# Kernel tuning notes

Hardware: AMD Instinct MI355X
Metric: run time of the kernel (lower is better)

Reference implementation:

```python
import jax, jax.numpy as jnp
import numpy as np

N, Wd = 1000000, 20
EPS = 1e-16


def setup_inputs() -> dict:
    key = jax.random.key(0)
    ks = jax.random.split(key, 40)
    def rn(i, shape, scale=0.05):
        return jax.random.normal(ks[i], shape, dtype=jnp.float32) * scale
    inp = {
        "X": rn(0, (1, 14), 1.0),
        "read_weights": jax.nn.sigmoid(rn(1, (1, N), 1.0)),
        "write_weights": jax.nn.sigmoid(rn(2, (1, N), 1.0)),
        "Memory": jnp.full((N, Wd), 1e-6, dtype=jnp.float32),
        "read_head": jax.nn.sigmoid(rn(3, (1, Wd), 1.0)),
        "W1": rn(4, (48, 14)), "b1": rn(5, (48,)),
        "W2": rn(6, (72, 48)), "b2": rn(7, (72,)),
        "Wxi": rn(8, ((Wd + 6) * 2 + 2 * Wd, 72)), "bxi": rn(9, ((Wd + 6) * 2 + 2 * Wd,)),
        "Wz": rn(10, (3, 72)), "bz": rn(11, (3,)),
        "Wv": rn(12, (20, 325)), "bv": rn(13, (20,)),
        "aW1": rn(14, (110, 40)), "ab1": rn(15, (110,)),
        "aW2": rn(16, (190, 110)), "ab2": rn(17, (190,)),
        "aW3": rn(18, (270, 190)), "ab3": rn(19, (270,)),
        "aW4": rn(20, (325, 270)), "ab4": rn(21, (325,)),
        "mW1": rn(22, (110, 40)), "mb1": rn(23, (110,)),
        "mW2": rn(24, (190, 110)), "mb2": rn(25, (190,)),
        "mW3": rn(26, (270, 190)), "mb3": rn(27, (270,)),
        "mW4": rn(28, (325, 270)), "mb4": rn(29, (325,)),
    }
    return inp


def _alu(x, W1, b1, W2, b2, W3, b3, W4, b4):
    x = jax.nn.relu(x @ W1.T + b1)
    x = jax.nn.relu(x @ W2.T + b2)
    x = jax.nn.relu(x @ W3.T + b3)
    return jax.nn.softmax(x @ W4.T + b4, axis=-1)


def _head_params(p):  # p: (1, Wd+6)
    k = jnp.tanh(p[0, :Wd])[None, :]              # (1, Wd)
    g = jax.nn.sigmoid(p[0, Wd])
    s = jax.nn.softmax(p[0, Wd + 1:Wd + 4])        # (3,)
    gamma = 1.0 + jax.nn.softplus(p[0, Wd + 4])
    beta = jax.nn.softplus(p[0, Wd + 5])
    return k, g, s, gamma, beta


def _address(Memory, k, beta, g, s, gamma, w_prev):
    Me = Memory + EPS                              # (N, Wd)
    ke = k + EPS                                   # (1, Wd)
    num = (Me @ ke.T)[:, 0]                        # (N,)
    den = jnp.maximum(jnp.linalg.norm(Me, axis=-1), 1e-8) * \
          jnp.maximum(jnp.linalg.norm(ke, axis=-1), 1e-8)
    w_c = jax.nn.softmax((num / den) * beta)       # (N,)
    w_g = g * w_c + (1.0 - g) * w_prev             # (1, N)
    pad = jnp.concatenate([w_g[:, -1:], w_g, w_g[:, :1]], axis=1)  # (1, N+2)
    w_r = s[0] * pad[:, :N] + s[1] * pad[:, 1:N + 1] + s[2] * pad[:, 2:]
    w = w_r ** gamma
    return w / (jnp.sum(w, axis=1, keepdims=True) + EPS)


def reference(X, read_weights, write_weights, Memory, read_head,
              W1, b1, W2, b2, Wxi, bxi, Wz, bz, Wv, bv,
              aW1, ab1, aW2, ab2, aW3, ab3, aW4, ab4,
              mW1, mb1, mW2, mb2, mW3, mb3, mW4, mb4):
    h = X @ W1.T + b1                # (1, 48)  (no activation, faithful)
    h = h @ W2.T + b2                # (1, 72)
    xi = h @ Wxi.T + bxi             # (1, 92)
    zeta = h @ Wz.T + bz             # (1, 3)

    rp = xi[0, :Wd + 6][None, :]
    wp = xi[0, Wd + 6:(Wd + 6) * 2][None, :]
    erase = jax.nn.sigmoid(xi[0, (Wd + 6) * 2:(Wd + 6) * 2 + Wd][None, :])
    add = jnp.tanh(xi[0, (Wd + 6) * 2 + Wd:(Wd + 6) * 2 + 2 * Wd][None, :])

    k, g, s, gamma, beta = _head_params(rp)
    rw = _address(Memory, k, beta, g, s, gamma, read_weights)
    k, g, s, gamma, beta = _head_params(wp)
    ww = _address(Memory, k, beta, g, s, gamma, write_weights)

    new_read_head = rw @ Memory                    # (1, Wd)
    alu_in = jnp.concatenate([read_head, new_read_head], axis=1)  # (1, 2*Wd)

    rho = jax.nn.sigmoid(zeta[0, 0])
    alu_head = jax.nn.softmax(zeta[:, 1:], axis=-1)  # (1, 2)
    out_add = _alu(alu_in, aW1, ab1, aW2, ab2, aW3, ab3, aW4, ab4)
    out_mul = _alu(alu_in, mW1, mb1, mW2, mb2, mW3, mb3, mW4, mb4)
    out = alu_head[0, 0] * out_add + alu_head[0, 1] * out_mul  # (1, 325)

    v = out @ Wv.T + bv                              # (1, 20)
    add = rho * add + (1.0 - rho) * v

    new_memory = Memory * (1.0 - ww.T @ erase) + ww.T @ add  # (N, Wd)
    return out, rw, ww, new_memory, new_read_head
```

## Files before the change

kernel.cpp:

```cpp
#include <hip/hip_runtime.h>
#include <math.h>

#define NN 1000000
#define NF4 5000000
#define WD 20
#define NB 977
#define PST 1024

#define OUT_OFF 0
#define RW_OFF  325
#define WW_OFF  1000325
#define NM_OFF  2000325
#define NRH_OFF 22000325

__device__ __forceinline__ float sigmoidf_(float x){ return 1.0f/(1.0f+expf(-x)); }
__device__ __forceinline__ float softplusf_(float x){ return (x>30.f)?x:log1pf(expf(x)); }

__global__ __launch_bounds__(256) void k_scores(
    const float* __restrict__ X,
    const float* __restrict__ W1, const float* __restrict__ b1,
    const float* __restrict__ W2, const float* __restrict__ b2,
    const float* __restrict__ Wxi, const float* __restrict__ bxi,
    const float* __restrict__ Wz, const float* __restrict__ bz,
    const float* __restrict__ M, float* __restrict__ Pg,
    float2* __restrict__ sc2, float4* __restrict__ pms){
  __shared__ float4 ld[1280];
  __shared__ float h1[48], h2[72], xi[95], sP[132];
  int t=threadIdx.x, b=blockIdx.x;
  if(t<48){ float a=b1[t]; const float* w=W1+t*14; for(int c=0;c<14;c++) a+=X[c]*w[c]; h1[t]=a; }
  __syncthreads();
  if(t<72){ float a=b2[t]; const float* w=W2+t*48; for(int c=0;c<48;c++) a+=h1[c]*w[c]; h2[t]=a; }
  __syncthreads();
  if(t<92){ float a=bxi[t]; const float* w=Wxi+t*72; for(int c=0;c<72;c++) a+=h2[c]*w[c]; xi[t]=a; }
  else if(t<95){ int z=t-92; float a=bz[z]; const float* w=Wz+z*72; for(int c=0;c<72;c++) a+=h2[c]*w[c]; xi[92+z]=a; }
  __syncthreads();
  if(t<20){
    sP[0+t]  = tanhf(xi[t]);
    sP[32+t] = tanhf(xi[26+t]);
    sP[64+t] = sigmoidf_(xi[52+t]);
    sP[84+t] = tanhf(xi[72+t]);
  }
  __syncthreads();
  if(t==32){
    float g=sigmoidf_(xi[20]);
    float a0=xi[21],a1=xi[22],a2=xi[23];
    float mx=fmaxf(a0,fmaxf(a1,a2));
    float e0=expf(a0-mx),e1=expf(a1-mx),e2=expf(a2-mx),es=e0+e1+e2;
    float gamma=1.0f+softplusf_(xi[24]);
    float beta=softplusf_(xi[25]);
    float n2=0.f;
#pragma unroll
    for(int j=0;j<20;j++){ float ke=sP[j]+1e-16f; n2+=ke*ke; }
    sP[20]=g; sP[21]=e0/es; sP[22]=e1/es; sP[23]=e2/es; sP[24]=gamma; sP[25]=beta;
    sP[26]=fmaxf(sqrtf(n2),1e-8f);
  }
  if(t==96){
    float g=sigmoidf_(xi[46]);
    float a0=xi[47],a1=xi[48],a2=xi[49];
    float mx=fmaxf(a0,fmaxf(a1,a2));
    float e0=expf(a0-mx),e1=expf(a1-mx),e2=expf(a2-mx),es=e0+e1+e2;
    float gamma=1.0f+softplusf_(xi[50]);
    float beta=softplusf_(xi[51]);
    float n2=0.f;
#pragma unroll
    for(int j=0;j<20;j++){ float ke=sP[32+j]+1e-16f; n2+=ke*ke; }
    sP[52]=g; sP[53]=e0/es; sP[54]=e1/es; sP[55]=e2/es; sP[56]=gamma; sP[57]=beta;
    sP[58]=fmaxf(sqrtf(n2),1e-8f);
  }
  if(t==160){
    sP[104]=sigmoidf_(xi[92]);
    float mx=fmaxf(xi[93],xi[94]);
    float e1=expf(xi[93]-mx), e2=expf(xi[94]-mx);
    sP[105]=e1/(e1+e2); sP[106]=e2/(e1+e2);
  }
  __syncthreads();
  if(b==0 && t<132) Pg[t]=sP[t];
  float kr[20], kw[20];
#pragma unroll
  for(int j=0;j<20;j++){ kr[j]=sP[j]+1e-16f; kw[j]=sP[32+j]+1e-16f; }
  float betar=sP[25], betaw=sP[57], knr=sP[26], knw=sP[58];
  const float4* Mf4=(const float4*)M;
  float sR[4], sW[4];
  for(int p=0;p<4;p++){
    int rb=b*1024+p*256;
    size_t f4b=(size_t)rb*5;
#pragma unroll
    for(int k=0;k<5;k++){
      size_t idx=f4b+(size_t)(k*256+t);
      ld[k*256+t] = (idx<NF4)?Mf4[idx]:make_float4(0.f,0.f,0.f,0.f);
    }
    __syncthreads();
    int i=rb+t;
    float srv=-3.0e38f, swv=-3.0e38f;
    if(i<NN){
      float dr=0.f,dw=0.f,n2=0.f;
#pragma unroll
      for(int q=0;q<5;q++){
        float4 v=ld[t*5+q];
        float m0=v.x+1e-16f,m1=v.y+1e-16f,m2=v.z+1e-16f,m3=v.w+1e-16f;
        dr+=m0*kr[4*q]+m1*kr[4*q+1]+m2*kr[4*q+2]+m3*kr[4*q+3];
        dw+=m0*kw[4*q]+m1*kw[4*q+1]+m2*kw[4*q+2]+m3*kw[4*q+3];
        n2+=m0*m0+m1*m1+m2*m2+m3*m3;
      }
      float nm=fmaxf(sqrtf(n2),1e-8f);
      srv=betar*(dr/(nm*knr));
      swv=betaw*(dw/(nm*knw));
      sc2[i]=make_float2(srv,swv);
    }
    sR[p]=srv; sW[p]=swv;
    __syncthreads();
  }
  float* r1=(float*)ld; float* r2=r1+256;
  double* d1=(double*)(r1+512); double* d2=d1+256;
  float lm1=fmaxf(fmaxf(sR[0],sR[1]),fmaxf(sR[2],sR[3]));
  float lm2=fmaxf(fmaxf(sW[0],sW[1]),fmaxf(sW[2],sW[3]));
  r1[t]=lm1; r2[t]=lm2; __syncthreads();
  for(int o=128;o>0;o>>=1){ if(t<o){ r1[t]=fmaxf(r1[t],r1[t+o]); r2[t]=fmaxf(r2[t],r2[t+o]); } __syncthreads(); }
  float mb1=r1[0], mb2=r2[0]; __syncthreads();
  double s1=0.0,s2=0.0;
#pragma unroll
  for(int p=0;p<4;p++){ s1+=(double)expf(sR[p]-mb1); s2+=(double)expf(sW[p]-mb2); }
  d1[t]=s1; d2[t]=s2; __syncthreads();
  for(int o=128;o>0;o>>=1){ if(t<o){ d1[t]+=d1[t+o]; d2[t]+=d2[t+o]; } __syncthreads(); }
  if(t==0) pms[b]=make_float4(mb1,mb2,(float)d1[0],(float)d2[0]);
}

__global__ __launch_bounds__(256) void k_shift(const float2* __restrict__ sc2,
                        const float* __restrict__ wpr, const float* __restrict__ wpw,
                        const float* __restrict__ M, const float* __restrict__ P,
                        const float4* __restrict__ pms,
                        float* __restrict__ w_r_out, float* __restrict__ w_w_out,
                        double* __restrict__ pZ, double* __restrict__ pnrhT){
  __shared__ float4 ld[1280];
  __shared__ float bmS[4];
  float* r1=(float*)ld; float* r2=r1+256;
  double* d1=(double*)(r1+512); double* d2=d1+256;
  float* wsum=(float*)(d2+256);
  int t=threadIdx.x, b=blockIdx.x;
  float4 v4[4];
#pragma unroll
  for(int k=0;k<4;k++){
    int idx=t+k*256;
    v4[k] = (idx<NB) ? pms[idx] : make_float4(-3.0e38f,-3.0e38f,0.f,0.f);
  }
  float lm1=fmaxf(fmaxf(v4[0].x,v4[1].x),fmaxf(v4[2].x,v4[3].x));
  float lm2=fmaxf(fmaxf(v4[0].y,v4[1].y),fmaxf(v4[2].y,v4[3].y));
  r1[t]=lm1; r2[t]=lm2; __syncthreads();
  for(int o=128;o>0;o>>=1){ if(t<o){ r1[t]=fmaxf(r1[t],r1[t+o]); r2[t]=fmaxf(r2[t],r2[t+o]); } __syncthreads(); }
  if(t==0){ bmS[0]=r1[0]; bmS[1]=r2[0]; } __syncthreads();
  float mr=bmS[0], mw=bmS[1];
  double s1=0.0,s2=0.0;
#pragma unroll
  for(int k=0;k<4;k++){
    s1 += (double)v4[k].z * (double)expf(v4[k].x-mr);
    s2 += (double)v4[k].w * (double)expf(v4[k].y-mw);
  }
  d1[t]=s1; d2[t]=s2; __syncthreads();
  for(int o=128;o>0;o>>=1){ if(t<o){ d1[t]+=d1[t+o]; d2[t]+=d2[t+o]; } __syncthreads(); }
  if(t==0){ bmS[2]=(float)d1[0]; bmS[3]=(float)d2[0]; } __syncthreads();
  float Sr=bmS[2], Sw=bmS[3];
  float gr=P[20], s0r=P[21], s1r=P[22], s2r=P[23], gar=P[24];
  float gw=P[52], s0w=P[53], s1w=P[54], s2w=P[55], gaw=P[56];
  float omgr=1.0f-gr, omgw=1.0f-gw;
  const float4* Mf4=(const float4*)M;
  float acc[20];
#pragma unroll
  for(int j=0;j<20;j++) acc[j]=0.f;
  double zr=0.0, zw=0.0;
  for(int p=0;p<4;p++){
    int rb=b*1024+p*256;
    size_t f4b=(size_t)rb*5;
#pragma unroll
    for(int k=0;k<5;k++){
      size_t idx=f4b+(size_t)(k*256+t);
      ld[k*256+t] = (idx<NF4)?Mf4[idx]:make_float4(0.f,0.f,0.f,0.f);
    }
    __syncthreads();
    int i=rb+t;
    if(i<NN){
      int im1=(i==0)?(NN-1):(i-1);
      int ip1=(i==NN-1)?0:(i+1);
      float2 scm=sc2[im1], sc0=sc2[i], scp=sc2[ip1];
      float wgrm = gr*(expf(scm.x-mr)/Sr) + omgr*wpr[im1];
      float wgr0 = gr*(expf(sc0.x-mr)/Sr) + omgr*wpr[i  ];
      float wgrp = gr*(expf(scp.x-mr)/Sr) + omgr*wpr[ip1];
      float wgwm = gw*(expf(scm.y-mw)/Sw) + omgw*wpw[im1];
      float wgw0 = gw*(expf(sc0.y-mw)/Sw) + omgw*wpw[i  ];
      float wgwp = gw*(expf(scp.y-mw)/Sw) + omgw*wpw[ip1];
      float wr = powf(s0r*wgrm + s1r*wgr0 + s2r*wgrp, gar);
      float ww = powf(s0w*wgwm + s1w*wgw0 + s2w*wgwp, gaw);
      w_r_out[i]=wr; w_w_out[i]=ww;
      zr+=(double)wr; zw+=(double)ww;
#pragma unroll
      for(int q=0;q<5;q++){
        float4 mv=ld[t*5+q];
        acc[4*q+0]+=wr*mv.x; acc[4*q+1]+=wr*mv.y; acc[4*q+2]+=wr*mv.z; acc[4*q+3]+=wr*mv.w;
      }
    }
    __syncthreads();
  }
  d1[t]=zr; d2[t]=zw; __syncthreads();
  for(int o=128;o>0;o>>=1){ if(t<o){ d1[t]+=d1[t+o]; d2[t]+=d2[t+o]; } __syncthreads(); }
  if(t==0){ pZ[2*b]=d1[0]; pZ[2*b+1]=d2[0]; }
  __syncthreads();
#pragma unroll
  for(int j=0;j<20;j++){
    for(int off=32;off>0;off>>=1) acc[j]+=__shfl_down(acc[j],off,64);
  }
  int wave=t>>6, lane=t&63;
  if(lane==0){
#pragma unroll
    for(int j=0;j<20;j++) wsum[wave*20+j]=acc[j];
  }
  __syncthreads();
  if(t<20){
    double s=(double)wsum[0*20+t]+(double)wsum[1*20+t]+(double)wsum[2*20+t]+(double)wsum[3*20+t];
    pnrhT[(size_t)t*PST+b]=s;
  }
}

__global__ __launch_bounds__(256) void k_l12(
    const double* __restrict__ pZ, const double* __restrict__ pnrhT,
    const float* __restrict__ read_head,
    const float* __restrict__ aW1,const float* __restrict__ ab1,
    const float* __restrict__ mW1,const float* __restrict__ mb1,
    const float* __restrict__ aW2,const float* __restrict__ ab2,
    const float* __restrict__ mW2,const float* __restrict__ mb2,
    float* __restrict__ out, float* __restrict__ h2g, double* __restrict__ Sd){
  __shared__ float in40[40], h1s[110];
  __shared__ double dred[24];
  int t=threadIdx.x, b=blockIdx.x, wave=t>>6, lane=t&63;
  int net=(b>=48);
  for(int j=wave; j<22; j+=4){
    double s=0.0;
    if(j<20){
      const double* src=pnrhT+(size_t)j*PST;
      for(int idx=lane; idx<NB; idx+=64) s+=src[idx];
    } else {
      for(int idx=lane; idx<NB; idx+=64) s+=pZ[2*idx+(j-20)];
    }
    for(int off=32;off>0;off>>=1) s+=__shfl_down(s,off,64);
    if(lane==0) dred[j]=s;
  }
  __syncthreads();
  if(t<20){
    double Zr=dred[20]+1e-16;
    float nv=(float)(dred[t]/Zr);
    in40[20+t]=nv; in40[t]=read_head[t];
    if(b==0) out[NRH_OFF+t]=nv;
  }
  if(b==0 && t==21){ Sd[0]=dred[20]; Sd[1]=dred[21]; }
  __syncthreads();
  int g=t>>4, l16=t&15;
  const float* W1=net?mW1:aW1; const float* B1=net?mb1:ab1;
  for(int pass=0; pass<7; ++pass){
    int r=pass*16+g;
    if(r<110){
      const float* w=W1+(size_t)r*40;
      float a=0.f;
      for(int c=l16;c<40;c+=16) a+=w[c]*in40[c];
      a+=__shfl_xor(a,8,64); a+=__shfl_xor(a,4,64); a+=__shfl_xor(a,2,64); a+=__shfl_xor(a,1,64);
      if(l16==0) h1s[r]=fmaxf(a+B1[r],0.f);
    }
  }
  __syncthreads();
  int r=(b-net*48)*4+wave;
  if(r<190){
    const float* w=(net?mW2:aW2)+(size_t)r*110;
    float a=0.f;
    for(int c=lane;c<110;c+=64) a+=w[c]*h1s[c];
    for(int off=32;off>0;off>>=1) a+=__shfl_down(a,off,64);
    if(lane==0) h2g[net*190+r]=fmaxf(a+(net?mb2:ab2)[r],0.f);
  }
}

__global__ __launch_bounds__(256) void k_l3(const float* __restrict__ h2g,
    const float* __restrict__ aW3,const float* __restrict__ ab3,
    const float* __restrict__ mW3,const float* __restrict__ mb3,
    float* __restrict__ h3g){
  int t=threadIdx.x, b=blockIdx.x, wave=t>>6, lane=t&63;
  int net=(b>=68);
  int r=(b-net*68)*4+wave;
  if(r>=270) return;
  const float* w=(net?mW3:aW3)+(size_t)r*190;
  const float* in=h2g+net*190;
  float a=0.f;
  for(int c=lane;c<190;c+=64) a+=w[c]*in[c];
  for(int off=32;off>0;off>>=1) a+=__shfl_down(a,off,64);
  if(lane==0) h3g[net*270+r]=fmaxf(a+(net?mb3:ab3)[r],0.f);
}

__global__ __launch_bounds__(256) void k_l4(const float* __restrict__ h3g,
    const float* __restrict__ aW4,const float* __restrict__ ab4,
    const float* __restrict__ mW4,const float* __restrict__ mb4,
    float* __restrict__ h4g){
  int t=threadIdx.x, b=blockIdx.x, wave=t>>6, lane=t&63;
  int net=(b>=82);
  int r=(b-net*82)*4+wave;
  if(r>=325) return;
  const float* w=(net?mW4:aW4)+(size_t)r*270;
  const float* in=h3g+net*270;
  float a=0.f;
  for(int c=lane;c<270;c+=64) a+=w[c]*in[c];
  for(int off=32;off>0;off>>=1) a+=__shfl_down(a,off,64);
  if(lane==0) h4g[net*325+r]=a+(net?mb4:ab4)[r];
}

__global__ __launch_bounds__(256) void k_fin(const float* __restrict__ h4g,
    const float* __restrict__ Wv, const float* __restrict__ bv,
    float* __restrict__ P, float* __restrict__ out){
  __shared__ float red[256], outv[325], sc[2];
  int t=threadIdx.x, b=blockIdx.x;
  float a0=h4g[t], a1=(t<69)?h4g[256+t]:-3.0e38f;
  red[t]=fmaxf(a0,a1); __syncthreads();
  for(int o=128;o>0;o>>=1){ if(t<o) red[t]=fmaxf(red[t],red[t+o]); __syncthreads(); }
  if(t==0) sc[0]=red[0]; __syncthreads();
  float ea0=expf(a0-sc[0]), ea1=(t<69)?expf(a1-sc[0]):0.f;
  red[t]=ea0+ea1; __syncthreads();
  for(int o=128;o>0;o>>=1){ if(t<o) red[t]+=red[t+o]; __syncthreads(); }
  if(t==0) sc[1]=red[0]; __syncthreads();
  float sA=sc[1];
  float pA0=ea0/sA, pA1=ea1/sA;
  __syncthreads();
  float m0=h4g[325+t], m1=(t<69)?h4g[325+256+t]:-3.0e38f;
  red[t]=fmaxf(m0,m1); __syncthreads();
  for(int o=128;o>0;o>>=1){ if(t<o) red[t]=fmaxf(red[t],red[t+o]); __syncthreads(); }
  if(t==0) sc[0]=red[0]; __syncthreads();
  float em0=expf(m0-sc[0]), em1=(t<69)?expf(m1-sc[0]):0.f;
  red[t]=em0+em1; __syncthreads();
  for(int o=128;o>0;o>>=1){ if(t<o) red[t]+=red[t+o]; __syncthreads(); }
  if(t==0) sc[1]=red[0]; __syncthreads();
  float sM=sc[1];
  float ah0=P[105], ah1=P[106];
  outv[t]=ah0*pA0+ah1*(em0/sM);
  if(t<69) outv[256+t]=ah0*pA1+ah1*(em1/sM);
  __syncthreads();
  if(b==20){
    out[OUT_OFF+t]=outv[t];
    if(t<69) out[OUT_OFF+256+t]=outv[256+t];
  } else {
    const float* w=Wv+(size_t)b*325;
    float a=w[t]*outv[t];
    if(t<69) a+=w[256+t]*outv[256+t];
    red[t]=a; __syncthreads();
    for(int o=128;o>0;o>>=1){ if(t<o) red[t]+=red[t+o]; __syncthreads(); }
    if(t==0){
      float rho=P[104];
      P[112+b]=rho*P[84+b]+(1.0f-rho)*(red[0]+bv[b]);
    }
  }
}

__global__ __launch_bounds__(256) void k_memupd(const float* __restrict__ M,
                         float* __restrict__ w_r, float* __restrict__ w_w,
                         const float* __restrict__ P, const double* __restrict__ Sd,
                         float* __restrict__ nm){
  __shared__ float4 ld[1280];
  int t=threadIdx.x, b=blockIdx.x;
  float er[20], af[20];
#pragma unroll
  for(int j=0;j<20;j++){ er[j]=P[64+j]; af[j]=P[112+j]; }
  float Zr=(float)Sd[0]+1e-16f, Zw=(float)Sd[1]+1e-16f;
  const float4* Mf4=(const float4*)M;
  float4* nmf4=(float4*)nm;
  for(int p=0;p<4;p++){
    int rb=b*1024+p*256;
    size_t f4b=(size_t)rb*5;
#pragma unroll
    for(int k=0;k<5;k++){
      size_t idx=f4b+(size_t)(k*256+t);
      if(idx<NF4) ld[k*256+t]=Mf4[idx];
    }
    __syncthreads();
    int i=rb+t;
    if(i<NN){
      float wrn=w_r[i]/Zr;
      float wwn=w_w[i]/Zw;
      w_r[i]=wrn; w_w[i]=wwn;
#pragma unroll
      for(int q=0;q<5;q++){
        float4 v=ld[t*5+q];
        float4 o;
        o.x=v.x*(1.0f-wwn*er[4*q+0])+wwn*af[4*q+0];
        o.y=v.y*(1.0f-wwn*er[4*q+1])+wwn*af[4*q+1];
        o.z=v.z*(1.0f-wwn*er[4*q+2])+wwn*af[4*q+2];
        o.w=v.w*(1.0f-wwn*er[4*q+3])+wwn*af[4*q+3];
        ld[t*5+q]=o;
      }
    }
    __syncthreads();
#pragma unroll
    for(int k=0;k<5;k++){
      size_t idx=f4b+(size_t)(k*256+t);
      if(idx<NF4) nmf4[idx]=ld[k*256+t];
    }
    __syncthreads();
  }
}

extern "C" void kernel_launch(void* const* d_in, const int* in_sizes, int n_in,
                              void* d_out, int out_size, void* d_ws, size_t ws_size,
                              hipStream_t stream) {
  const float* X    =(const float*)d_in[0];
  const float* rwp  =(const float*)d_in[1];
  const float* wwp  =(const float*)d_in[2];
  const float* Mem  =(const float*)d_in[3];
  const float* rhd  =(const float*)d_in[4];
  const float* W1   =(const float*)d_in[5];
  const float* b1   =(const float*)d_in[6];
  const float* W2   =(const float*)d_in[7];
  const float* b2   =(const float*)d_in[8];
  const float* Wxi  =(const float*)d_in[9];
  const float* bxi  =(const float*)d_in[10];
  const float* Wz   =(const float*)d_in[11];
  const float* bz   =(const float*)d_in[12];
  const float* Wv   =(const float*)d_in[13];
  const float* bv   =(const float*)d_in[14];
  const float* aW1  =(const float*)d_in[15];
  const float* ab1  =(const float*)d_in[16];
  const float* aW2  =(const float*)d_in[17];
  const float* ab2  =(const float*)d_in[18];
  const float* aW3  =(const float*)d_in[19];
  const float* ab3  =(const float*)d_in[20];
  const float* aW4  =(const float*)d_in[21];
  const float* ab4  =(const float*)d_in[22];
  const float* mW1  =(const float*)d_in[23];
  const float* mb1  =(const float*)d_in[24];
  const float* mW2  =(const float*)d_in[25];
  const float* mb2  =(const float*)d_in[26];
  const float* mW3  =(const float*)d_in[27];
  const float* mb3  =(const float*)d_in[28];
  const float* mW4  =(const float*)d_in[29];
  const float* mb4  =(const float*)d_in[30];

  float* out = (float*)d_out;
  char* ws = (char*)d_ws;
  float*  P   = (float*)(ws + 0);
  double* Sd  = (double*)(ws + 2048);
  float*  h2g = (float*)(ws + 4096);
  float*  h3g = (float*)(ws + 8192);
  float*  h4g = (float*)(ws + 12288);
  float4* pms = (float4*)(ws + 16384);
  double* pZ  = (double*)(ws + 65536);
  double* pnrhT=(double*)(ws + 131072);

  float2* sc2 = (float2*)(out + NM_OFF);
  float*  w_r = out + RW_OFF;
  float*  w_w = out + WW_OFF;
  float*  nm  = out + NM_OFF;

  k_scores<<<NB,256,0,stream>>>(X,W1,b1,W2,b2,Wxi,bxi,Wz,bz,Mem,P,sc2,pms);
  k_shift<<<NB,256,0,stream>>>(sc2,rwp,wwp,Mem,P,pms,w_r,w_w,pZ,pnrhT);
  k_l12<<<96,256,0,stream>>>(pZ,pnrhT,rhd,aW1,ab1,mW1,mb1,aW2,ab2,mW2,mb2,out,h2g,Sd);
  k_l3<<<136,256,0,stream>>>(h2g,aW3,ab3,mW3,mb3,h3g);
  k_l4<<<164,256,0,stream>>>(h3g,aW4,ab4,mW4,mb4,h4g);
  k_fin<<<21,256,0,stream>>>(h4g,Wv,bv,P,out);
  k_memupd<<<NB,256,0,stream>>>(Mem,w_r,w_w,P,Sd,nm);
}
```

Baseline: 130.5 us.

## Fuse small MLP kernels into one cooperative kernel with grid syncs

Replaces the four small kernels (l12, l3, l4, fin) with a single cooperative kernel of 160 blocks that uses grid.sync between layers. This targets the launch overhead and inter-kernel gaps on the serial tail of the computation. It also spreads the first-layer work and the reductions across more waves. Grid-wide barriers carry their own cost, and layer 4 now loops over 650 rows with 640 waves.

After: 193.0 us. 48.0% more time.

```diff
diff --git a/kernel.cpp b/kernel.cpp
--- a/kernel.cpp
+++ b/kernel.cpp
@@ -1,11 +1,15 @@
 #include <hip/hip_runtime.h>
+#include <hip/hip_cooperative_groups.h>
 #include <math.h>
+
+namespace cg = cooperative_groups;
 
 #define NN 1000000
 #define NF4 5000000
 #define WD 20
 #define NB 977
 #define PST 1024
+#define CB 160
 
 #define OUT_OFF 0
 #define RW_OFF  325
@@ -219,134 +223,124 @@
   }
 }
 
-__global__ __launch_bounds__(256) void k_l12(
+__global__ __launch_bounds__(256) void k_coop(
     const double* __restrict__ pZ, const double* __restrict__ pnrhT,
-    const float* __restrict__ read_head,
+    const float* __restrict__ rhd,
     const float* __restrict__ aW1,const float* __restrict__ ab1,
     const float* __restrict__ mW1,const float* __restrict__ mb1,
     const float* __restrict__ aW2,const float* __restrict__ ab2,
     const float* __restrict__ mW2,const float* __restrict__ mb2,
-    float* __restrict__ out, float* __restrict__ h2g, double* __restrict__ Sd){
-  __shared__ float in40[40], h1s[110];
-  __shared__ double dred[24];
-  int t=threadIdx.x, b=blockIdx.x, wave=t>>6, lane=t&63;
-  int net=(b>=48);
-  for(int j=wave; j<22; j+=4){
-    double s=0.0;
-    if(j<20){
-      const double* src=pnrhT+(size_t)j*PST;
-      for(int idx=lane; idx<NB; idx+=64) s+=src[idx];
-    } else {
-      for(int idx=lane; idx<NB; idx+=64) s+=pZ[2*idx+(j-20)];
-    }
-    for(int off=32;off>0;off>>=1) s+=__shfl_down(s,off,64);
-    if(lane==0) dred[j]=s;
-  }
-  __syncthreads();
-  if(t<20){
-    double Zr=dred[20]+1e-16;
-    float nv=(float)(dred[t]/Zr);
-    in40[20+t]=nv; in40[t]=read_head[t];
-    if(b==0) out[NRH_OFF+t]=nv;
-  }
-  if(b==0 && t==21){ Sd[0]=dred[20]; Sd[1]=dred[21]; }
-  __syncthreads();
-  int g=t>>4, l16=t&15;
-  const float* W1=net?mW1:aW1; const float* B1=net?mb1:ab1;
-  for(int pass=0; pass<7; ++pass){
-    int r=pass*16+g;
-    if(r<110){
-      const float* w=W1+(size_t)r*40;
-      float a=0.f;
-      for(int c=l16;c<40;c+=16) a+=w[c]*in40[c];
-      a+=__shfl_xor(a,8,64); a+=__shfl_xor(a,4,64); a+=__shfl_xor(a,2,64); a+=__shfl_xor(a,1,64);
-      if(l16==0) h1s[r]=fmaxf(a+B1[r],0.f);
-    }
-  }
-  __syncthreads();
-  int r=(b-net*48)*4+wave;
-  if(r<190){
-    const float* w=(net?mW2:aW2)+(size_t)r*110;
-    float a=0.f;
-    for(int c=lane;c<110;c+=64) a+=w[c]*h1s[c];
-    for(int off=32;off>0;off>>=1) a+=__shfl_down(a,off,64);
-    if(lane==0) h2g[net*190+r]=fmaxf(a+(net?mb2:ab2)[r],0.f);
-  }
-}
-
-__global__ __launch_bounds__(256) void k_l3(const float* __restrict__ h2g,
     const float* __restrict__ aW3,const float* __restrict__ ab3,
     const float* __restrict__ mW3,const float* __restrict__ mb3,
-    float* __restrict__ h3g){
-  int t=threadIdx.x, b=blockIdx.x, wave=t>>6, lane=t&63;
-  int net=(b>=68);
-  int r=(b-net*68)*4+wave;
-  if(r>=270) return;
-  const float* w=(net?mW3:aW3)+(size_t)r*190;
-  const float* in=h2g+net*190;
-  float a=0.f;
-  for(int c=lane;c<190;c+=64) a+=w[c]*in[c];
-  for(int off=32;off>0;off>>=1) a+=__shfl_down(a,off,64);
-  if(lane==0) h3g[net*270+r]=fmaxf(a+(net?mb3:ab3)[r],0.f);
-}
-
-__global__ __launch_bounds__(256) void k_l4(const float* __restrict__ h3g,
     const float* __restrict__ aW4,const float* __restrict__ ab4,
     const float* __restrict__ mW4,const float* __restrict__ mb4,
-    float* __restrict__ h4g){
+    const float* __restrict__ Wv, const float* __restrict__ bv,
+    float* __restrict__ P, float* __restrict__ out,
+    double* __restrict__ Sd, double* __restrict__ nrhraw,
+    float* __restrict__ h1g, float* __restrict__ h2g,
+    float* __restrict__ h3g, float* __restrict__ h4g){
+  cg::grid_group grid = cg::this_grid();
+  __shared__ double dd[256];
+  __shared__ float in40[40];
+  __shared__ float red[256], sc[2];
   int t=threadIdx.x, b=blockIdx.x, wave=t>>6, lane=t&63;
-  int net=(b>=82);
-  int r=(b-net*82)*4+wave;
-  if(r>=325) return;
-  const float* w=(net?mW4:aW4)+(size_t)r*270;
-  const float* in=h3g+net*270;
-  float a=0.f;
-  for(int c=lane;c<270;c+=64) a+=w[c]*in[c];
-  for(int off=32;off>0;off>>=1) a+=__shfl_down(a,off,64);
-  if(lane==0) h4g[net*325+r]=a+(net?mb4:ab4)[r];
-}
-
-__global__ __launch_bounds__(256) void k_fin(const float* __restrict__ h4g,
-    const float* __restrict__ Wv, const float* __restrict__ bv,
-    float* __restrict__ P, float* __restrict__ out){
-  __shared__ float red[256], outv[325], sc[2];
-  int t=threadIdx.x, b=blockIdx.x;
-  float a0=h4g[t], a1=(t<69)?h4g[256+t]:-3.0e38f;
-  red[t]=fmaxf(a0,a1); __syncthreads();
-  for(int o=128;o>0;o>>=1){ if(t<o) red[t]=fmaxf(red[t],red[t+o]); __syncthreads(); }
-  if(t==0) sc[0]=red[0]; __syncthreads();
-  float ea0=expf(a0-sc[0]), ea1=(t<69)?expf(a1-sc[0]):0.f;
-  red[t]=ea0+ea1; __syncthreads();
-  for(int o=128;o>0;o>>=1){ if(t<o) red[t]+=red[t+o]; __syncthreads(); }
-  if(t==0) sc[1]=red[0]; __syncthreads();
-  float sA=sc[1];
-  float pA0=ea0/sA, pA1=ea1/sA;
-  __syncthreads();
-  float m0=h4g[325+t], m1=(t<69)?h4g[325+256+t]:-3.0e38f;
-  red[t]=fmaxf(m0,m1); __syncthreads();
-  for(int o=128;o>0;o>>=1){ if(t<o) red[t]=fmaxf(red[t],red[t+o]); __syncthreads(); }
-  if(t==0) sc[0]=red[0]; __syncthreads();
-  float em0=expf(m0-sc[0]), em1=(t<69)?expf(m1-sc[0]):0.f;
-  red[t]=em0+em1; __syncthreads();
-  for(int o=128;o>0;o>>=1){ if(t<o) red[t]+=red[t+o]; __syncthreads(); }
-  if(t==0) sc[1]=red[0]; __syncthreads();
-  float sM=sc[1];
-  float ah0=P[105], ah1=P[106];
-  outv[t]=ah0*pA0+ah1*(em0/sM);
-  if(t<69) outv[256+t]=ah0*pA1+ah1*(em1/sM);
-  __syncthreads();
-  if(b==20){
-    out[OUT_OFF+t]=outv[t];
-    if(t<69) out[OUT_OFF+256+t]=outv[256+t];
-  } else {
-    const float* w=Wv+(size_t)b*325;
-    float a=w[t]*outv[t];
-    if(t<69) a+=w[256+t]*outv[256+t];
-    red[t]=a; __syncthreads();
+  int wid=b*4+wave;
+  if(b<20){
+    const double* src=pnrhT+(size_t)b*PST;
+    double s=0.0;
+    for(int idx=t; idx<NB; idx+=256) s+=src[idx];
+    dd[t]=s; __syncthreads();
+    for(int o=128;o>0;o>>=1){ if(t<o) dd[t]+=dd[t+o]; __syncthreads(); }
+    if(t==0) nrhraw[b]=dd[0];
+  } else if(b==20||b==21){
+    int c=b-20;
+    double s=0.0;
+    for(int idx=t; idx<NB; idx+=256) s+=pZ[2*idx+c];
+    dd[t]=s; __syncthreads();
+    for(int o=128;o>0;o>>=1){ if(t<o) dd[t]+=dd[t+o]; __syncthreads(); }
+    if(t==0) Sd[c]=dd[0];
+  }
+  grid.sync();
+  if(t<40){
+    in40[t]=(t<20)? rhd[t] : (float)(nrhraw[t-20]/(Sd[0]+1e-16));
+  }
+  if(b==0 && t<20) out[NRH_OFF+t]=(float)(nrhraw[t]/(Sd[0]+1e-16));
+  __syncthreads();
+  if(wid<220){
+    int net=(wid>=110), r=wid-net*110;
+    const float* w=(net?mW1:aW1)+(size_t)r*40;
+    float a=(lane<40)? w[lane]*in40[lane] : 0.f;
+    for(int off=32;off>0;off>>=1) a+=__shfl_down(a,off,64);
+    if(lane==0) h1g[wid]=fmaxf(a+(net?mb1:ab1)[r],0.f);
+  }
+  grid.sync();
+  if(wid<380){
+    int net=(wid>=190), r=wid-net*190;
+    const float* w=(net?mW2:aW2)+(size_t)r*110;
+    const float* in=h1g+net*110;
+    float a=0.f;
+    for(int c=lane;c<110;c+=64) a+=w[c]*in[c];
+    for(int off=32;off>0;off>>=1) a+=__shfl_down(a,off,64);
+    if(lane==0) h2g[wid]=fmaxf(a+(net?mb2:ab2)[r],0.f);
+  }
+  grid.sync();
+  if(wid<540){
+    int net=(wid>=270), r=wid-net*270;
+    const float* w=(net?mW3:aW3)+(size_t)r*190;
+    const float* in=h2g+net*190;
+    float a=0.f;
+    for(int c=lane;c<190;c+=64) a+=w[c]*in[c];
+    for(int off=32;off>0;off>>=1) a+=__shfl_down(a,off,64);
+    if(lane==0) h3g[wid]=fmaxf(a+(net?mb3:ab3)[r],0.f);
+  }
+  grid.sync();
+  for(int r0=wid; r0<650; r0+=CB*4){
+    int net=(r0>=325), r=r0-net*325;
+    const float* w=(net?mW4:aW4)+(size_t)r*270;
+    const float* in=h3g+net*270;
+    float a=0.f;
+    for(int c=lane;c<270;c+=64) a+=w[c]*in[c];
+    for(int off=32;off>0;off>>=1) a+=__shfl_down(a,off,64);
+    if(lane==0) h4g[r0]=a+(net?mb4:ab4)[r];
+  }
+  grid.sync();
+  if(b<21){
+    float a0=h4g[t], a1=(t<69)?h4g[256+t]:-3.0e38f;
+    red[t]=fmaxf(a0,a1); __syncthreads();
+    for(int o=128;o>0;o>>=1){ if(t<o) red[t]=fmaxf(red[t],red[t+o]); __syncthreads(); }
+    if(t==0) sc[0]=red[0]; __syncthreads();
+    float ea0=expf(a0-sc[0]), ea1=(t<69)?expf(a1-sc[0]):0.f;
+    red[t]=ea0+ea1; __syncthreads();
     for(int o=128;o>0;o>>=1){ if(t<o) red[t]+=red[t+o]; __syncthreads(); }
-    if(t==0){
-      float rho=P[104];
-      P[112+b]=rho*P[84+b]+(1.0f-rho)*(red[0]+bv[b]);
+    if(t==0) sc[1]=red[0]; __syncthreads();
+    float sA=sc[1];
+    float pA0=ea0/sA, pA1=ea1/sA;
+    __syncthreads();
+    float m0=h4g[325+t], m1=(t<69)?h4g[325+256+t]:-3.0e38f;
+    red[t]=fmaxf(m0,m1); __syncthreads();
+    for(int o=128;o>0;o>>=1){ if(t<o) red[t]=fmaxf(red[t],red[t+o]); __syncthreads(); }
+    if(t==0) sc[0]=red[0]; __syncthreads();
+    float em0=expf(m0-sc[0]), em1=(t<69)?expf(m1-sc[0]):0.f;
+    red[t]=em0+em1; __syncthreads();
+    for(int o=128;o>0;o>>=1){ if(t<o) red[t]+=red[t+o]; __syncthreads(); }
+    if(t==0) sc[1]=red[0]; __syncthreads();
+    float sM=sc[1];
+    float ah0=P[105], ah1=P[106];
+    float ov0=ah0*pA0+ah1*(em0/sM);
+    float ov1=(t<69)? ah0*pA1+ah1*(em1/sM) : 0.f;
+    if(b==20){
+      out[OUT_OFF+t]=ov0;
+      if(t<69) out[OUT_OFF+256+t]=ov1;
+    } else {
+      const float* w=Wv+(size_t)b*325;
+      float a=w[t]*ov0;
+      if(t<69) a+=w[256+t]*ov1;
+      red[t]=a; __syncthreads();
+      for(int o=128;o>0;o>>=1){ if(t<o) red[t]+=red[t+o]; __syncthreads(); }
+      if(t==0){
+        float rho=P[104];
+        P[112+b]=rho*P[84+b]+(1.0f-rho)*(red[0]+bv[b]);
+      }
     }
   }
 }
@@ -435,14 +429,16 @@
 
   float* out = (float*)d_out;
   char* ws = (char*)d_ws;
-  float*  P   = (float*)(ws + 0);
-  double* Sd  = (double*)(ws + 2048);
-  float*  h2g = (float*)(ws + 4096);
-  float*  h3g = (float*)(ws + 8192);
-  float*  h4g = (float*)(ws + 12288);
-  float4* pms = (float4*)(ws + 16384);
-  double* pZ  = (double*)(ws + 65536);
-  double* pnrhT=(double*)(ws + 131072);
+  float*  P      = (float*)(ws + 0);
+  double* Sd     = (double*)(ws + 2048);
+  double* nrhraw = (double*)(ws + 2304);
+  float*  h1g    = (float*)(ws + 4096);
+  float*  h2g    = (float*)(ws + 8192);
+  float*  h3g    = (float*)(ws + 12288);
+  float*  h4g    = (float*)(ws + 16384);
+  float4* pms    = (float4*)(ws + 32768);
+  double* pZ     = (double*)(ws + 65536);
+  double* pnrhT  = (double*)(ws + 131072);
 
   float2* sc2 = (float2*)(out + NM_OFF);
   float*  w_r = out + RW_OFF;
@@ -451,9 +447,18 @@
 
   k_scores<<<NB,256,0,stream>>>(X,W1,b1,W2,b2,Wxi,bxi,Wz,bz,Mem,P,sc2,pms);
   k_shift<<<NB,256,0,stream>>>(sc2,rwp,wwp,Mem,P,pms,w_r,w_w,pZ,pnrhT);
-  k_l12<<<96,256,0,stream>>>(pZ,pnrhT,rhd,aW1,ab1,mW1,mb1,aW2,ab2,mW2,mb2,out,h2g,Sd);
-  k_l3<<<136,256,0,stream>>>(h2g,aW3,ab3,mW3,mb3,h3g);
-  k_l4<<<164,256,0,stream>>>(h3g,aW4,ab4,mW4,mb4,h4g);
-  k_fin<<<21,256,0,stream>>>(h4g,Wv,bv,P,out);
+  {
+    void* args[] = {
+      (void*)&pZ,(void*)&pnrhT,(void*)&rhd,
+      (void*)&aW1,(void*)&ab1,(void*)&mW1,(void*)&mb1,
+      (void*)&aW2,(void*)&ab2,(void*)&mW2,(void*)&mb2,
+      (void*)&aW3,(void*)&ab3,(void*)&mW3,(void*)&mb3,
+      (void*)&aW4,(void*)&ab4,(void*)&mW4,(void*)&mb4,
+      (void*)&Wv,(void*)&bv,(void*)&P,(void*)&out,
+      (void*)&Sd,(void*)&nrhraw,
+      (void*)&h1g,(void*)&h2g,(void*)&h3g,(void*)&h4g
+    };
+    hipLaunchCooperativeKernel((void*)k_coop, dim3(CB), dim3(256), args, 0, stream);
+  }
   k_memupd<<<NB,256,0,stream>>>(Mem,w_r,w_w,P,Sd,nm);
 }
```

## Fuse reductions via last-block tickets and prefetch ALU weights into cache

Applied to the files above, without the earlier changes.

The column reduction of the read-head and normaliser partials moves out of k_l12 into the last-finishing block of k_shift, found with an atomic ticket counter. k_l4 and k_fin are merged the same way, so the final softmax and Wv projection run in the last block of k_l4fin. That removes one launch and repeated reduction work across k_l12 blocks. Blocks 100-199 of k_scores also touch every ALU and Wv weight line to warm the cache for the small MLP kernels that follow. The cost is serial tail work in a single block, plus extra loads inside the memory-bound scoring kernel.

Measured after the change: 189.0 us. +44.8%, slower.

```diff
diff --git a/kernel.cpp b/kernel.cpp
--- a/kernel.cpp
+++ b/kernel.cpp
@@ -12,6 +12,8 @@
 #define WW_OFF  1000325
 #define NM_OFF  2000325
 #define NRH_OFF 22000325
+
+typedef unsigned int uint;
 
 __device__ __forceinline__ float sigmoidf_(float x){ return 1.0f/(1.0f+expf(-x)); }
 __device__ __forceinline__ float softplusf_(float x){ return (x>30.f)?x:log1pf(expf(x)); }
@@ -23,10 +25,17 @@
     const float* __restrict__ Wxi, const float* __restrict__ bxi,
     const float* __restrict__ Wz, const float* __restrict__ bz,
     const float* __restrict__ M, float* __restrict__ Pg,
-    float2* __restrict__ sc2, float4* __restrict__ pms){
+    float2* __restrict__ sc2, float4* __restrict__ pms,
+    uint* __restrict__ tk,
+    const float* __restrict__ aW1, const float* __restrict__ mW1,
+    const float* __restrict__ aW2, const float* __restrict__ mW2,
+    const float* __restrict__ aW3, const float* __restrict__ mW3,
+    const float* __restrict__ aW4, const float* __restrict__ mW4,
+    const float* __restrict__ Wv){
   __shared__ float4 ld[1280];
   __shared__ float h1[48], h2[72], xi[95], sP[132];
   int t=threadIdx.x, b=blockIdx.x;
+  if(b==0 && t<2) tk[t]=0u;
   if(t<48){ float a=b1[t]; const float* w=W1+t*14; for(int c=0;c<14;c++) a+=X[c]*w[c]; h1[t]=a; }
   __syncthreads();
   if(t<72){ float a=b2[t]; const float* w=W2+t*48; for(int c=0;c<48;c++) a+=h1[c]*w[c]; h2[t]=a; }
@@ -75,6 +84,21 @@
   }
   __syncthreads();
   if(b==0 && t<132) Pg[t]=sP[t];
+  if(b>=100 && b<200){
+    int pid=(b-100)*256+t;
+    float pf=0.f;
+    const float4* a4;
+    a4=(const float4*)aW1; for(int i=pid;i<1100;i+=25600)  pf+=a4[i].x;
+    a4=(const float4*)mW1; for(int i=pid;i<1100;i+=25600)  pf+=a4[i].x;
+    a4=(const float4*)aW2; for(int i=pid;i<5225;i+=25600)  pf+=a4[i].x;
+    a4=(const float4*)mW2; for(int i=pid;i<5225;i+=25600)  pf+=a4[i].x;
+    a4=(const float4*)aW3; for(int i=pid;i<12825;i+=25600) pf+=a4[i].x;
+    a4=(const float4*)mW3; for(int i=pid;i<12825;i+=25600) pf+=a4[i].x;
+    a4=(const float4*)aW4; for(int i=pid;i<21937;i+=25600) pf+=a4[i].x;
+    a4=(const float4*)mW4; for(int i=pid;i<21937;i+=25600) pf+=a4[i].x;
+    a4=(const float4*)Wv;  for(int i=pid;i<1625;i+=25600)  pf+=a4[i].x;
+    if(pf==12345.678f) Pg[255]=pf;
+  }
   float kr[20], kw[20];
 #pragma unroll
   for(int j=0;j<20;j++){ kr[j]=sP[j]+1e-16f; kw[j]=sP[32+j]+1e-16f; }
@@ -129,10 +153,15 @@
                         const float* __restrict__ wpr, const float* __restrict__ wpw,
                         const float* __restrict__ M, const float* __restrict__ P,
                         const float4* __restrict__ pms,
+                        const float* __restrict__ read_head,
                         float* __restrict__ w_r_out, float* __restrict__ w_w_out,
-                        double* __restrict__ pZ, double* __restrict__ pnrhT){
+                        double* __restrict__ pZ, double* __restrict__ pnrhT,
+                        double* __restrict__ Sd, float* __restrict__ in40g,
+                        float* __restrict__ out, uint* __restrict__ tk){
   __shared__ float4 ld[1280];
   __shared__ float bmS[4];
+  __shared__ int lastFlag;
+  __shared__ double colr[22];
   float* r1=(float*)ld; float* r2=r1+256;
   double* d1=(double*)(r1+512); double* d2=d1+256;
   float* wsum=(float*)(d2+256);
@@ -217,39 +246,48 @@
     double s=(double)wsum[0*20+t]+(double)wsum[1*20+t]+(double)wsum[2*20+t]+(double)wsum[3*20+t];
     pnrhT[(size_t)t*PST+b]=s;
   }
-}
-
-__global__ __launch_bounds__(256) void k_l12(
-    const double* __restrict__ pZ, const double* __restrict__ pnrhT,
-    const float* __restrict__ read_head,
+  __syncthreads();
+  if(t==0){
+    __threadfence();
+    uint old=__hip_atomic_fetch_add(tk,1u,__ATOMIC_ACQ_REL,__HIP_MEMORY_SCOPE_AGENT);
+    lastFlag=(old==NB-1);
+  }
+  __syncthreads();
+  if(lastFlag){
+    __threadfence();
+    for(int j=wave;j<22;j+=4){
+      double s=0.0;
+      if(j<20){
+        const double* src=pnrhT+(size_t)j*PST;
+        for(int idx=lane;idx<NB;idx+=64) s+=src[idx];
+      } else {
+        int c=j-20;
+        for(int idx=lane;idx<NB;idx+=64) s+=pZ[2*idx+c];
+      }
+      for(int off=32;off>0;off>>=1) s+=__shfl_down(s,off,64);
+      if(lane==0) colr[j]=s;
+    }
+    __syncthreads();
+    if(t<20){
+      double Zr=colr[20]+1e-16;
+      float nv=(float)(colr[t]/Zr);
+      in40g[20+t]=nv; in40g[t]=read_head[t];
+      out[NRH_OFF+t]=nv;
+    }
+    if(t==20){ Sd[0]=colr[20]; Sd[1]=colr[21]; }
+  }
+}
+
+__global__ __launch_bounds__(256) void k_l12(const float* __restrict__ in40g,
     const float* __restrict__ aW1,const float* __restrict__ ab1,
     const float* __restrict__ mW1,const float* __restrict__ mb1,
     const float* __restrict__ aW2,const float* __restrict__ ab2,
     const float* __restrict__ mW2,const float* __restrict__ mb2,
-    float* __restrict__ out, float* __restrict__ h2g, double* __restrict__ Sd){
+    float* __restrict__ h2g){
   __shared__ float in40[40], h1s[110];
-  __shared__ double dred[24];
   int t=threadIdx.x, b=blockIdx.x, wave=t>>6, lane=t&63;
   int net=(b>=48);
-  for(int j=wave; j<22; j+=4){
-    double s=0.0;
-    if(j<20){
-      const double* src=pnrhT+(size_t)j*PST;
-      for(int idx=lane; idx<NB; idx+=64) s+=src[idx];
-    } else {
-      for(int idx=lane; idx<NB; idx+=64) s+=pZ[2*idx+(j-20)];
-    }
-    for(int off=32;off>0;off>>=1) s+=__shfl_down(s,off,64);
-    if(lane==0) dred[j]=s;
-  }
-  __syncthreads();
-  if(t<20){
-    double Zr=dred[20]+1e-16;
-    float nv=(float)(dred[t]/Zr);
-    in40[20+t]=nv; in40[t]=read_head[t];
-    if(b==0) out[NRH_OFF+t]=nv;
-  }
-  if(b==0 && t==21){ Sd[0]=dred[20]; Sd[1]=dred[21]; }
+  if(t<40) in40[t]=in40g[t];
   __syncthreads();
   int g=t>>4, l16=t&15;
   const float* W1=net?mW1:aW1; const float* B1=net?mb1:ab1;
@@ -290,27 +328,34 @@
   if(lane==0) h3g[net*270+r]=fmaxf(a+(net?mb3:ab3)[r],0.f);
 }
 
-__global__ __launch_bounds__(256) void k_l4(const float* __restrict__ h3g,
+__global__ __launch_bounds__(256) void k_l4fin(const float* __restrict__ h3g,
     const float* __restrict__ aW4,const float* __restrict__ ab4,
     const float* __restrict__ mW4,const float* __restrict__ mb4,
-    float* __restrict__ h4g){
+    const float* __restrict__ Wv, const float* __restrict__ bv,
+    float* __restrict__ h4g, float* __restrict__ P, float* __restrict__ out,
+    uint* __restrict__ tk){
+  __shared__ float red[256], outv[325], sc[2];
+  __shared__ int lastFlag;
   int t=threadIdx.x, b=blockIdx.x, wave=t>>6, lane=t&63;
-  int net=(b>=82);
-  int r=(b-net*82)*4+wave;
-  if(r>=325) return;
-  const float* w=(net?mW4:aW4)+(size_t)r*270;
-  const float* in=h3g+net*270;
-  float a=0.f;
-  for(int c=lane;c<270;c+=64) a+=w[c]*in[c];
-  for(int off=32;off>0;off>>=1) a+=__shfl_down(a,off,64);
-  if(lane==0) h4g[net*325+r]=a+(net?mb4:ab4)[r];
-}
-
-__global__ __launch_bounds__(256) void k_fin(const float* __restrict__ h4g,
-    const float* __restrict__ Wv, const float* __restrict__ bv,
-    float* __restrict__ P, float* __restrict__ out){
-  __shared__ float red[256], outv[325], sc[2];
-  int t=threadIdx.x, b=blockIdx.x;
+  int wid=b*4+wave;
+  if(wid<650){
+    int net=(wid>=325), r=wid-net*325;
+    const float* w=(net?mW4:aW4)+(size_t)r*270;
+    const float* in=h3g+net*270;
+    float a=0.f;
+    for(int c=lane;c<270;c+=64) a+=w[c]*in[c];
+    for(int off=32;off>0;off>>=1) a+=__shfl_down(a,off,64);
+    if(lane==0) h4g[wid]=a+(net?mb4:ab4)[r];
+  }
+  __syncthreads();
+  if(t==0){
+    __threadfence();
+    uint old=__hip_atomic_fetch_add(tk,1u,__ATOMIC_ACQ_REL,__HIP_MEMORY_SCOPE_AGENT);
+    lastFlag=(old==163u);
+  }
+  __syncthreads();
+  if(!lastFlag) return;
+  __threadfence();
   float a0=h4g[t], a1=(t<69)?h4g[256+t]:-3.0e38f;
   red[t]=fmaxf(a0,a1); __syncthreads();
   for(int o=128;o>0;o>>=1){ if(t<o) red[t]=fmaxf(red[t],red[t+o]); __syncthreads(); }
@@ -332,22 +377,17 @@
   if(t==0) sc[1]=red[0]; __syncthreads();
   float sM=sc[1];
   float ah0=P[105], ah1=P[106];
-  outv[t]=ah0*pA0+ah1*(em0/sM);
-  if(t<69) outv[256+t]=ah0*pA1+ah1*(em1/sM);
-  __syncthreads();
-  if(b==20){
-    out[OUT_OFF+t]=outv[t];
-    if(t<69) out[OUT_OFF+256+t]=outv[256+t];
-  } else {
-    const float* w=Wv+(size_t)b*325;
-    float a=w[t]*outv[t];
-    if(t<69) a+=w[256+t]*outv[256+t];
-    red[t]=a; __syncthreads();
-    for(int o=128;o>0;o>>=1){ if(t<o) red[t]+=red[t+o]; __syncthreads(); }
-    if(t==0){
-      float rho=P[104];
-      P[112+b]=rho*P[84+b]+(1.0f-rho)*(red[0]+bv[b]);
-    }
+  float ov0=ah0*pA0+ah1*(em0/sM);
+  outv[t]=ov0; out[OUT_OFF+t]=ov0;
+  if(t<69){ float ov1=ah0*pA1+ah1*(em1/sM); outv[256+t]=ov1; out[OUT_OFF+256+t]=ov1; }
+  __syncthreads();
+  float rho=P[104];
+  for(int r=wave; r<20; r+=4){
+    const float* w=Wv+(size_t)r*325;
+    float a=0.f;
+    for(int c=lane;c<325;c+=64) a+=w[c]*outv[c];
+    for(int off=32;off>0;off>>=1) a+=__shfl_down(a,off,64);
+    if(lane==0) P[112+r]=rho*P[84+r]+(1.0f-rho)*(a+bv[r]);
   }
 }
 
@@ -435,25 +475,28 @@
 
   float* out = (float*)d_out;
   char* ws = (char*)d_ws;
-  float*  P   = (float*)(ws + 0);
-  double* Sd  = (double*)(ws + 2048);
-  float*  h2g = (float*)(ws + 4096);
-  float*  h3g = (float*)(ws + 8192);
-  float*  h4g = (float*)(ws + 12288);
-  float4* pms = (float4*)(ws + 16384);
-  double* pZ  = (double*)(ws + 65536);
-  double* pnrhT=(double*)(ws + 131072);
+  float*  P     = (float*)(ws + 0);
+  double* Sd    = (double*)(ws + 2048);
+  float*  in40g = (float*)(ws + 2304);
+  uint*   tk    = (uint*)(ws + 2560);
+  float*  h2g   = (float*)(ws + 4096);
+  float*  h3g   = (float*)(ws + 8192);
+  float*  h4g   = (float*)(ws + 12288);
+  float4* pms   = (float4*)(ws + 32768);
+  double* pZ    = (double*)(ws + 65536);
+  double* pnrhT = (double*)(ws + 131072);
 
   float2* sc2 = (float2*)(out + NM_OFF);
   float*  w_r = out + RW_OFF;
   float*  w_w = out + WW_OFF;
   float*  nm  = out + NM_OFF;
 
-  k_scores<<<NB,256,0,stream>>>(X,W1,b1,W2,b2,Wxi,bxi,Wz,bz,Mem,P,sc2,pms);
-  k_shift<<<NB,256,0,stream>>>(sc2,rwp,wwp,Mem,P,pms,w_r,w_w,pZ,pnrhT);
-  k_l12<<<96,256,0,stream>>>(pZ,pnrhT,rhd,aW1,ab1,mW1,mb1,aW2,ab2,mW2,mb2,out,h2g,Sd);
+  k_scores<<<NB,256,0,stream>>>(X,W1,b1,W2,b2,Wxi,bxi,Wz,bz,Mem,P,sc2,pms,tk,
+                                aW1,mW1,aW2,mW2,aW3,mW3,aW4,mW4,Wv);
+  k_shift<<<NB,256,0,stream>>>(sc2,rwp,wwp,Mem,P,pms,rhd,w_r,w_w,pZ,pnrhT,
+                               Sd,in40g,out,tk);
+  k_l12<<<96,256,0,stream>>>(in40g,aW1,ab1,mW1,mb1,aW2,ab2,mW2,mb2,h2g);
   k_l3<<<136,256,0,stream>>>(h2g,aW3,ab3,mW3,mb3,h3g);
-  k_l4<<<164,256,0,stream>>>(h3g,aW4,ab4,mW4,mb4,h4g);
-  k_fin<<<21,256,0,stream>>>(h4g,Wv,bv,P,out);
+  k_l4fin<<<164,256,0,stream>>>(h3g,aW4,ab4,mW4,mb4,Wv,bv,h4g,P,out,tk+1);
   k_memupd<<<NB,256,0,stream>>>(Mem,w_r,w_w,P,Sd,nm);
 }
```
